# Kernel optimization log

Hardware: AMD Instinct MI355X
Metric: run time of the kernel (lower is better)

The kernel has to match this reference:

```python
import jax, jax.numpy as jnp
import numpy as np

# Model dims (match init_kwargs)
N_P, NV, P, S = 60, 5, 20, 14   # particles, vertices, pf features, sv features
HID, DE, DO, NCLS, BATCH = 60, 20, 24, 2, 512

# Rr/Rs one-hot matrices encode edges (r, s) for r != s with r varying slowest.
# So gather-by-Rr == repeat each node N-1 times, gather-by-Rs == index by senders,
# and scatter-sum by Rr^T == reshape to [B, N, N-1, De] and sum axis 2.
_SENDERS = np.array([s for r in range(N_P) for s in range(N_P) if s != r])


def _lin_params(key, din, dout):
    kw, kb = jax.random.split(key)
    bound = 1.0 / np.sqrt(din)
    w = jax.random.uniform(kw, (din, dout), minval=-bound, maxval=bound, dtype=jnp.float32)
    b = jax.random.uniform(kb, (dout,), minval=-bound, maxval=bound, dtype=jnp.float32)
    return w, b


def setup_inputs() -> dict:
    key = jax.random.key(0)
    ks = jax.random.split(key, 12)
    inp = {
        'x': jax.random.normal(ks[0], (BATCH, P, N_P), dtype=jnp.float32),
        'y': jax.random.normal(ks[1], (BATCH, S, NV), dtype=jnp.float32),
    }
    specs = [('fr', [(2 * P, HID), (HID, HID), (HID, DE)]),
             ('pv', [(S + P, HID), (HID, HID), (HID, DE)]),
             ('fo', [(P + 2 * DE, HID), (HID, HID), (HID, DO)])]
    ki = 2
    for name, dims in specs:
        for j, (di, do) in enumerate(dims, 1):
            w, b = _lin_params(ks[ki], di, do)
            ki += 1
            inp[f'{name}_w{j}'] = w
            inp[f'{name}_b{j}'] = b
    w, b = _lin_params(ks[11], DO, NCLS)
    inp['fc_w'] = w
    inp['fc_b'] = b
    return inp


def _mlp3(h, w1, b1, w2, b2, w3, b3):
    h = jax.nn.relu(h @ w1 + b1)
    h = jax.nn.relu(h @ w2 + b2)
    return jax.nn.relu(h @ w3 + b3)


def reference(x, y, fr_w1, fr_b1, fr_w2, fr_b2, fr_w3, fr_b3,
              pv_w1, pv_b1, pv_w2, pv_b2, pv_w3, pv_b3,
              fo_w1, fo_b1, fo_w2, fo_b2, fo_w3, fo_b3, fc_w, fc_b):
    xt = jnp.swapaxes(x, -1, -2)  # [B, N, P]
    yt = jnp.swapaxes(y, -1, -2)  # [B, Nv, S]
    B = xt.shape[0]

    # particle-particle edge conv (gather via index, scatter-sum via reshape)
    Orr = jnp.repeat(xt, N_P - 1, axis=1)          # [B, Nr, P], receiver features
    Ors = xt[:, _SENDERS]                          # [B, Nr, P], sender features
    E = _mlp3(jnp.concatenate([Orr, Ors], axis=-1),
              fr_w1, fr_b1, fr_w2, fr_b2, fr_w3, fr_b3)  # [B, Nr, De]
    Ebar_pp = E.reshape(B, N_P, N_P - 1, DE).sum(axis=2)  # [B, N, De]

    # particle-vertex edge conv (Rk repeats particles, Rv tiles vertices)
    Ork = jnp.repeat(xt, NV, axis=1)               # [B, Nt, P]
    Orv = jnp.tile(yt, (1, N_P, 1))                # [B, Nt, S]
    E2 = _mlp3(jnp.concatenate([Ork, Orv], axis=-1),
               pv_w1, pv_b1, pv_w2, pv_b2, pv_w3, pv_b3)  # [B, Nt, De]
    Ebar_pv = E2.reshape(B, N_P, NV, DE).sum(axis=2)      # [B, N, De]

    C = jnp.concatenate([xt, Ebar_pp, Ebar_pv], axis=-1)  # [B, N, P + 2*De]
    O = _mlp3(C, fo_w1, fo_b1, fo_w2, fo_b2, fo_w3, fo_b3)  # [B, N, Do]
    return O.sum(axis=-2) @ fc_w + fc_b  # [B, num_classes]
```

## Files before the change

### kernel.cpp

```cpp
#include <hip/hip_runtime.h>

#define BATCH 512
#define NPART 60
#define PFEAT 20
#define SFEAT 14
#define NVTX  5
#define HID   60
#define DE    20
#define DO    24
#define NCLS  2
#define SR    68

typedef _Float16 half8  __attribute__((ext_vector_type(8)));
typedef _Float16 half4v __attribute__((ext_vector_type(4)));
typedef __fp16   fp16x2 __attribute__((ext_vector_type(2)));
typedef float    f32x4  __attribute__((ext_vector_type(4)));

__device__ __forceinline__ half4v pkcvt4(f32x4 a) {
    fp16x2 lo = __builtin_amdgcn_cvt_pkrtz(a[0], a[1]);
    fp16x2 hi = __builtin_amdgcn_cvt_pkrtz(a[2], a[3]);
    half4v r;
    r[0] = (_Float16)lo[0]; r[1] = (_Float16)lo[1];
    r[2] = (_Float16)hi[0]; r[3] = (_Float16)hi[1];
    return r;
}
__device__ __forceinline__ half4v relu4(half4v a) {
#pragma unroll
    for (int j = 0; j < 4; ++j)
        a[j] = (a[j] > (_Float16)0.f) ? a[j] : (_Float16)0.f;
    return a;
}
__device__ __forceinline__ f32x4 bias4(const float* b, int col4, int lim) {
    f32x4 z = {0.f, 0.f, 0.f, 0.f};
    return (col4 < lim) ? *(const f32x4*)(b + col4) : z;
}

__global__ __launch_bounds__(256) void prep_kernel(
    const float* __restrict__ x,
    const float* __restrict__ fr_w1, const float* __restrict__ pv_w1,
    const float* __restrict__ fr_w2, const float* __restrict__ fr_w3,
    const float* __restrict__ pv_w2, const float* __restrict__ pv_w3,
    const float* __restrict__ fo_w1, const float* __restrict__ fo_w2,
    const float* __restrict__ fo_w3,
    _Float16* __restrict__ frW2p, _Float16* __restrict__ frW3p16,
    _Float16* __restrict__ pvW2p, _Float16* __restrict__ pvW3p16,
    _Float16* __restrict__ foW1p, _Float16* __restrict__ foW2p16,
    _Float16* __restrict__ foW3p16,
    _Float16* __restrict__ frW1Ap, _Float16* __restrict__ frW1Bp,
    _Float16* __restrict__ pvW1Ap, _Float16* __restrict__ xp)
{
    if (blockIdx.x < 16) {
        int idx = blockIdx.x*256 + threadIdx.x;
        {
            int j  = idx & 7;
            int L  = (idx >> 3) & 63;
            int kk = (idx >> 9) & 1;
            int u  = idx >> 10;
            int k  = kk*32 + (L >> 4)*8 + j;
            int n  = u*16 + (L & 15);
            bool ok = (k < HID && n < HID);
            frW2p[idx] = (_Float16)(ok ? fr_w2[k*HID + n] : 0.f);
            pvW2p[idx] = (_Float16)(ok ? pv_w2[k*HID + n] : 0.f);
            foW1p[idx] = (_Float16)(ok ? fo_w1[k*HID + n] : 0.f);
        }
        {
            int j  = idx & 3;
            int L  = (idx >> 2) & 63;
            int kt = (idx >> 8) & 3;
            int u  = idx >> 10;
            int k  = kt*16 + (L >> 4)*4 + j;
            int n  = u*16 + (L & 15);
            foW2p16[idx] = (_Float16)((k < HID && n < HID) ? fo_w2[k*HID + n] : 0.f);
        }
        if (idx < 2048) {
            {
                int j  = idx & 3;
                int L  = (idx >> 2) & 63;
                int kt = (idx >> 8) & 3;
                int u  = idx >> 10;
                int k  = kt*16 + (L >> 4)*4 + j;
                int n  = u*16 + (L & 15);
                frW3p16[idx] = (_Float16)((k < HID && n < DE) ? fr_w3[k*DE + n] : 0.f);
                pvW3p16[idx] = (_Float16)((k < HID && n < DE) ? pv_w3[k*DE + n] : 0.f);
                foW3p16[idx] = (_Float16)((k < HID && n < DO) ? fo_w3[k*DO + n] : 0.f);
            }
            {
                int j = idx & 7;
                int L = (idx >> 3) & 63;
                int u = idx >> 9;
                int k = (L >> 4)*8 + j;
                int n = u*16 + (L & 15);
                bool ok = (k < PFEAT && n < HID);
                frW1Ap[idx] = (_Float16)(ok ? fr_w1[k*HID + n] : 0.f);
                frW1Bp[idx] = (_Float16)(ok ? fr_w1[(PFEAT + k)*HID + n] : 0.f);
                pvW1Ap[idx] = (_Float16)(ok ? pv_w1[k*HID + n] : 0.f);
            }
        }
    } else {
        int idx = (blockIdx.x - 16)*256 + threadIdx.x;
        if (idx < BATCH*NPART*4) {
            int p = idx % NPART;
            int t = idx / NPART;
            int q = t & 3;
            int b = t >> 2;
            half8 v;
#pragma unroll
            for (int j = 0; j < 8; ++j) {
                int k = q*8 + j;
                v[j] = (_Float16)((k < PFEAT) ? x[((size_t)b*PFEAT + k)*NPART + p] : 0.f);
            }
            *(half8*)(xp + (size_t)idx*8) = v;
        }
    }
}

__global__ __launch_bounds__(512) void fused_kernel(
    const float* __restrict__ y,
    const float* __restrict__ fr_b1,
    const float* __restrict__ fr_b2, const float* __restrict__ fr_b3,
    const float* __restrict__ pv_w1, const float* __restrict__ pv_b1,
    const float* __restrict__ pv_b2, const float* __restrict__ pv_b3,
    const float* __restrict__ fo_b1, const float* __restrict__ fo_b2,
    const float* __restrict__ fo_b3,
    const float* __restrict__ fcw, const float* __restrict__ fcb,
    const half8*  __restrict__ frw2p, const half4v* __restrict__ frw3p16,
    const half8*  __restrict__ pvw2p, const half4v* __restrict__ pvw3p16,
    const half8*  __restrict__ fow1p, const half4v* __restrict__ fow2p16,
    const half4v* __restrict__ fow3p16,
    const half8*  __restrict__ frw1ap, const half8* __restrict__ frw1bp,
    const half8*  __restrict__ pvw1ap, const _Float16* __restrict__ xp,
    float* __restrict__ out)
{
    __shared__ __align__(16) _Float16 sFrA[NPART*SR];
    __shared__ __align__(16) _Float16 sFrB[NPART*SR];
    __shared__ __align__(16) _Float16 sPvA[NPART*SR];
    __shared__ __align__(16) _Float16 sPvV[NVTX*64];
    __shared__ __align__(16) _Float16 sEpp[NPART*DE];
    __shared__ __align__(16) _Float16 sEpvP[NVTX*NPART*DE];
    __shared__ __align__(16) float    sDsum[4][DO];
    __shared__ __align__(16) float    sBias[7*64];
    _Float16* sCin = sFrA;

    int bb   = blockIdx.x;
    int wv   = threadIdx.x >> 6;
    int lane = threadIdx.x & 63;
    int ml   = lane & 15;
    int q    = lane >> 4;

    {
        if (threadIdx.x < 448) {
            int arr = wv, i = lane;
            float bv = 0.f;
            if      (arr == 0) { if (i < HID) bv = fr_b2[i]; }
            else if (arr == 1) { if (i < DE)  bv = fr_b3[i]; }
            else if (arr == 2) { if (i < HID) bv = pv_b2[i]; }
            else if (arr == 3) { if (i < DE)  bv = pv_b3[i]; }
            else if (arr == 4) { if (i < HID) bv = fo_b1[i]; }
            else if (arr == 5) { if (i < HID) bv = fo_b2[i]; }
            else               { if (i < DO)  bv = fo_b3[i]; }
            sBias[threadIdx.x] = bv;
        }

        int tile = wv & 3;
        int row  = 16*tile + ml;
        int rr   = (row < NPART) ? row : 0;
        half8 bX = *(const half8*)(xp + (((size_t)bb*4 + q)*NPART + rr)*8);
#pragma unroll
        for (int task = 0; task < 2; ++task) {
            const half8* Wt; const float* bset; _Float16* Ot;
            if (wv < 4) {
                if (task == 0) { Wt = frw1ap; bset = fr_b1;  Ot = sFrA; }
                else           { Wt = pvw1ap; bset = nullptr; Ot = sPvA; }
            } else {
                if (task == 1) break;
                Wt = frw1bp; bset = nullptr; Ot = sFrB;
            }
#pragma unroll
            for (int u = 0; u < 4; ++u) {
                half8 w8 = Wt[u*64 + lane];
                f32x4 acc = bset ? bias4(bset, u*16 + 4*q, HID - 3)
                                 : (f32x4){0.f, 0.f, 0.f, 0.f};
                acc = __builtin_amdgcn_mfma_f32_16x16x32_f16(w8, bX, acc, 0, 0, 0);
                if (row < NPART)
                    *(half4v*)(Ot + row*SR + u*16 + 4*q) = pkcvt4(acc);
            }
        }
        for (int idx = threadIdx.x; idx < NVTX*64; idx += 512) {
            int v = idx >> 6;
            int h = idx & 63;
            float a = 0.f;
            if (h < HID) {
                a = pv_b1[h];
#pragma unroll
                for (int f = 0; f < SFEAT; ++f)
                    a += y[((size_t)bb*SFEAT + f)*NVTX + v] * pv_w1[(PFEAT + f)*HID + h];
            }
            sPvV[idx] = (_Float16)a;
        }
    }
    __syncthreads();

    {
        half8  w2r[8];
        half4v w3r[8];
#pragma unroll
        for (int t = 0; t < 8; ++t) w2r[t] = frw2p[t*64 + lane];
#pragma unroll
        for (int t = 0; t < 8; ++t) w3r[t] = frw3p16[t*64 + lane];
#pragma unroll
        for (int t = 0; t < 8; ++t) {
            asm volatile("" : "+v"(w2r[t]));
            asm volatile("" : "+v"(w3r[t]));
        }

        for (int r = wv; r < NPART; r += 8) {
            half8 u8k0 = *(const half8*)(sFrA + r*SR + q*8);
            half8 u8k1 = *(const half8*)(sFrA + r*SR + 32 + q*8);
            float s[2][4];
#pragma unroll
            for (int v = 0; v < 2; ++v)
#pragma unroll
                for (int i = 0; i < 4; ++i) s[v][i] = 0.f;

#pragma unroll
            for (int th = 0; th < 2; ++th) {
                half8 bA[2][2];
                float okf[2];
#pragma unroll
                for (int tl = 0; tl < 2; ++tl) {
                    int edge = 16*(2*th + tl) + ml;
                    bool eok = (edge < NPART-1);
                    okf[tl] = eok ? 1.f : 0.f;
                    int sr = eok ? (edge + (edge >= r)) : 0;
#pragma unroll
                    for (int kk = 0; kk < 2; ++kk) {
                        half8 v8 = *(const half8*)(sFrB + sr*SR + kk*32 + q*8);
                        half8 s8 = (kk ? u8k1 : u8k0) + v8;
#pragma unroll
                        for (int j = 0; j < 8; ++j) {
                            _Float16 vj = s8[j];
                            s8[j] = (vj > (_Float16)0.f) ? vj : (_Float16)0.f;
                        }
                        bA[tl][kk] = s8;
                    }
                }
                f32x4 acc3[2][2];
#pragma unroll
                for (int v = 0; v < 2; ++v) {
                    f32x4 bi = *(const f32x4*)(sBias + 1*64 + v*16 + 4*q);
#pragma unroll
                    for (int tl = 0; tl < 2; ++tl) acc3[v][tl] = bi;
                }
#pragma unroll
                for (int u = 0; u < 4; ++u) {
                    half8 w0 = w2r[u*2 + 0];
                    half8 w1 = w2r[u*2 + 1];
                    f32x4 bi2 = *(const f32x4*)(sBias + 0*64 + u*16 + 4*q);
                    half4v a3u[2];
#pragma unroll
                    for (int tl = 0; tl < 2; ++tl) {
                        f32x4 a = bi2;
                        a = __builtin_amdgcn_mfma_f32_16x16x32_f16(w0, bA[tl][0], a, 0, 0, 0);
                        a = __builtin_amdgcn_mfma_f32_16x16x32_f16(w1, bA[tl][1], a, 0, 0, 0);
                        a3u[tl] = relu4(pkcvt4(a));
                    }
                    half4v w3a = w3r[0*4 + u];
                    half4v w3b = w3r[1*4 + u];
#pragma unroll
                    for (int tl = 0; tl < 2; ++tl) {
                        acc3[0][tl] = __builtin_amdgcn_mfma_f32_16x16x16f16(w3a, a3u[tl], acc3[0][tl], 0, 0, 0);
                        acc3[1][tl] = __builtin_amdgcn_mfma_f32_16x16x16f16(w3b, a3u[tl], acc3[1][tl], 0, 0, 0);
                    }
                }
#pragma unroll
                for (int v = 0; v < 2; ++v)
#pragma unroll
                    for (int tl = 0; tl < 2; ++tl)
#pragma unroll
                        for (int i = 0; i < 4; ++i)
                            s[v][i] = fmaf(fmaxf(acc3[v][tl][i], 0.f), okf[tl], s[v][i]);
            }
#pragma unroll
            for (int v = 0; v < 2; ++v) {
#pragma unroll
                for (int i = 0; i < 4; ++i) {
                    s[v][i] += __shfl_xor(s[v][i], 1);
                    s[v][i] += __shfl_xor(s[v][i], 2);
                    s[v][i] += __shfl_xor(s[v][i], 4);
                    s[v][i] += __shfl_xor(s[v][i], 8);
                }
                int col4 = v*16 + 4*q;
                if (ml == 0 && col4 < DE) {
                    f32x4 o = {s[v][0], s[v][1], s[v][2], s[v][3]};
                    *(half4v*)(sEpp + r*DE + col4) = pkcvt4(o);
                }
            }
        }
    }

    if (wv < NVTX) {
        int gv = wv;
        half8  w2r[8];
        half4v w3r[8];
#pragma unroll
        for (int t = 0; t < 8; ++t) w2r[t] = pvw2p[t*64 + lane];
#pragma unroll
        for (int t = 0; t < 8; ++t) w3r[t] = pvw3p16[t*64 + lane];
#pragma unroll
        for (int t = 0; t < 8; ++t) {
            asm volatile("" : "+v"(w2r[t]));
            asm volatile("" : "+v"(w3r[t]));
        }
        half8 u8k0 = *(const half8*)(sPvV + gv*64 + q*8);
        half8 u8k1 = *(const half8*)(sPvV + gv*64 + 32 + q*8);
#pragma unroll
        for (int th = 0; th < 2; ++th) {
            half8 bA[2][2];
#pragma unroll
            for (int tl = 0; tl < 2; ++tl) {
                int p = 16*(2*th + tl) + ml;
                int sr = (p < NPART) ? p : 0;
#pragma unroll
                for (int kk = 0; kk < 2; ++kk) {
                    half8 v8 = *(const half8*)(sPvA + sr*SR + kk*32 + q*8);
                    half8 s8 = (kk ? u8k1 : u8k0) + v8;
#pragma unroll
                    for (int j = 0; j < 8; ++j) {
                        _Float16 vj = s8[j];
                        s8[j] = (vj > (_Float16)0.f) ? vj : (_Float16)0.f;
                    }
                    bA[tl][kk] = s8;
                }
            }
            f32x4 acc3[2][2];
#pragma unroll
            for (int v = 0; v < 2; ++v) {
                f32x4 bi = *(const f32x4*)(sBias + 3*64 + v*16 + 4*q);
#pragma unroll
                for (int tl = 0; tl < 2; ++tl) acc3[v][tl] = bi;
            }
#pragma unroll
            for (int u = 0; u < 4; ++u) {
                half8 w0 = w2r[u*2 + 0];
                half8 w1 = w2r[u*2 + 1];
                f32x4 bi2 = *(const f32x4*)(sBias + 2*64 + u*16 + 4*q);
                half4v a3u[2];
#pragma unroll
                for (int tl = 0; tl < 2; ++tl) {
                    f32x4 a = bi2;
                    a = __builtin_amdgcn_mfma_f32_16x16x32_f16(w0, bA[tl][0], a, 0, 0, 0);
                    a = __builtin_amdgcn_mfma_f32_16x16x32_f16(w1, bA[tl][1], a, 0, 0, 0);
                    a3u[tl] = relu4(pkcvt4(a));
                }
                half4v w3a = w3r[0*4 + u];
                half4v w3b = w3r[1*4 + u];
#pragma unroll
                for (int tl = 0; tl < 2; ++tl) {
                    acc3[0][tl] = __builtin_amdgcn_mfma_f32_16x16x16f16(w3a, a3u[tl], acc3[0][tl], 0, 0, 0);
                    acc3[1][tl] = __builtin_amdgcn_mfma_f32_16x16x16f16(w3b, a3u[tl], acc3[1][tl], 0, 0, 0);
                }
            }
#pragma unroll
            for (int v = 0; v < 2; ++v) {
                int col4 = v*16 + 4*q;
#pragma unroll
                for (int tl = 0; tl < 2; ++tl) {
                    int p = 16*(2*th + tl) + ml;
                    if (p < NPART && col4 < DE) {
                        half4v hv = relu4(pkcvt4(acc3[v][tl]));
                        *(half4v*)(sEpvP + (gv*NPART + p)*DE + col4) = hv;
                    }
                }
            }
        }
    }
    __syncthreads();

    for (int idx = threadIdx.x; idx < NPART*64; idx += 512) {
        int p = idx >> 6;
        int k = idx & 63;
        _Float16 v;
        if (k < PFEAT) {
            v = xp[(((size_t)bb*4 + (k >> 3))*NPART + p)*8 + (k & 7)];
        } else if (k < PFEAT + DE) {
            v = sEpp[p*DE + (k - PFEAT)];
        } else if (k < PFEAT + 2*DE) {
            int c = k - PFEAT - DE;
            float s = 0.f;
#pragma unroll
            for (int g5 = 0; g5 < NVTX; ++g5)
                s += (float)sEpvP[(g5*NPART + p)*DE + c];
            v = (_Float16)s;
        } else {
            v = (_Float16)0.f;
        }
        sCin[p*SR + k] = v;
    }
    __syncthreads();

    if (wv < 4) {
        int p = 16*wv + ml;
        int sp = (p < NPART) ? p : 0;
        half8 bC[2];
#pragma unroll
        for (int kk = 0; kk < 2; ++kk)
            bC[kk] = *(const half8*)(sCin + sp*SR + kk*32 + q*8);

        f32x4 acc1[4];
#pragma unroll
        for (int u = 0; u < 4; ++u) {
            acc1[u] = *(const f32x4*)(sBias + 4*64 + u*16 + 4*q);
            acc1[u] = __builtin_amdgcn_mfma_f32_16x16x32_f16(fow1p[(u*2 + 0)*64 + lane], bC[0], acc1[u], 0, 0, 0);
            acc1[u] = __builtin_amdgcn_mfma_f32_16x16x32_f16(fow1p[(u*2 + 1)*64 + lane], bC[1], acc1[u], 0, 0, 0);
        }
        half4v a2[4];
#pragma unroll
        for (int u = 0; u < 4; ++u) a2[u] = relu4(pkcvt4(acc1[u]));

        f32x4 acc2[4];
#pragma unroll
        for (int u = 0; u < 4; ++u) {
            acc2[u] = *(const f32x4*)(sBias + 5*64 + u*16 + 4*q);
#pragma unroll
            for (int kt = 0; kt < 4; ++kt)
                acc2[u] = __builtin_amdgcn_mfma_f32_16x16x16f16(fow2p16[(u*4 + kt)*64 + lane], a2[kt], acc2[u], 0, 0, 0);
        }
        half4v a3[4];
#pragma unroll
        for (int u = 0; u < 4; ++u) a3[u] = relu4(pkcvt4(acc2[u]));

        f32x4 acc3[2];
#pragma unroll
        for (int v = 0; v < 2; ++v) {
            acc3[v] = *(const f32x4*)(sBias + 6*64 + v*16 + 4*q);
#pragma unroll
            for (int u = 0; u < 4; ++u)
                acc3[v] = __builtin_amdgcn_mfma_f32_16x16x16f16(fow3p16[(v*4 + u)*64 + lane], a3[u], acc3[v], 0, 0, 0);
        }
#pragma unroll
        for (int v = 0; v < 2; ++v) {
            float s[4];
            bool ok = p < NPART;
#pragma unroll
            for (int i = 0; i < 4; ++i)
                s[i] = ok ? fmaxf(acc3[v][i], 0.f) : 0.f;
#pragma unroll
            for (int i = 0; i < 4; ++i) {
                s[i] += __shfl_xor(s[i], 1);
                s[i] += __shfl_xor(s[i], 2);
                s[i] += __shfl_xor(s[i], 4);
                s[i] += __shfl_xor(s[i], 8);
            }
            int col4 = v*16 + 4*q;
            if (ml == 0 && col4 < DO) {
                f32x4 o = {s[0], s[1], s[2], s[3]};
                *(f32x4*)(sDsum[wv] + col4) = o;
            }
        }
    }
    __syncthreads();

    if (wv == 0) {
        float tot = 0.f;
        if (lane < DO) {
#pragma unroll
            for (int w4 = 0; w4 < 4; ++w4) tot += sDsum[w4][lane];
        }
        float p0 = (lane < DO) ? tot * fcw[lane*NCLS + 0] : 0.f;
        float p1 = (lane < DO) ? tot * fcw[lane*NCLS + 1] : 0.f;
#pragma unroll
        for (int d = 1; d <= 16; d <<= 1) {
            p0 += __shfl_xor(p0, d);
            p1 += __shfl_xor(p1, d);
        }
        if (lane == 0) {
            out[bb*NCLS + 0] = p0 + fcb[0];
            out[bb*NCLS + 1] = p1 + fcb[1];
        }
    }
}

extern "C" void kernel_launch(void* const* d_in, const int* in_sizes, int n_in,
                              void* d_out, int out_size, void* d_ws, size_t ws_size,
                              hipStream_t stream)
{
    const float* x     = (const float*)d_in[0];
    const float* y     = (const float*)d_in[1];
    const float* fr_w1 = (const float*)d_in[2];
    const float* fr_b1 = (const float*)d_in[3];
    const float* fr_w2 = (const float*)d_in[4];
    const float* fr_b2 = (const float*)d_in[5];
    const float* fr_w3 = (const float*)d_in[6];
    const float* fr_b3 = (const float*)d_in[7];
    const float* pv_w1 = (const float*)d_in[8];
    const float* pv_b1 = (const float*)d_in[9];
    const float* pv_w2 = (const float*)d_in[10];
    const float* pv_b2 = (const float*)d_in[11];
    const float* pv_w3 = (const float*)d_in[12];
    const float* pv_b3 = (const float*)d_in[13];
    const float* fo_w1 = (const float*)d_in[14];
    const float* fo_b1 = (const float*)d_in[15];
    const float* fo_w2 = (const float*)d_in[16];
    const float* fo_b2 = (const float*)d_in[17];
    const float* fo_w3 = (const float*)d_in[18];
    const float* fo_b3 = (const float*)d_in[19];
    const float* fc_w  = (const float*)d_in[20];
    const float* fc_b  = (const float*)d_in[21];
    float* out = (float*)d_out;

    char* wsb = (char*)d_ws;
    size_t off = 0;
    auto alloc = [&](size_t bytes) { char* p = wsb + off; off += (bytes + 255) & ~(size_t)255; return p; };

    _Float16* frW2p   = (_Float16*)alloc(4096*2);
    _Float16* frW3p16 = (_Float16*)alloc(2048*2);
    _Float16* pvW2p   = (_Float16*)alloc(4096*2);
    _Float16* pvW3p16 = (_Float16*)alloc(2048*2);
    _Float16* foW1p   = (_Float16*)alloc(4096*2);
    _Float16* foW2p16 = (_Float16*)alloc(4096*2);
    _Float16* foW3p16 = (_Float16*)alloc(2048*2);
    _Float16* frW1Ap  = (_Float16*)alloc(2048*2);
    _Float16* frW1Bp  = (_Float16*)alloc(2048*2);
    _Float16* pvW1Ap  = (_Float16*)alloc(2048*2);
    _Float16* xp      = (_Float16*)alloc((size_t)BATCH*NPART*32*2);

    int xblocks = (BATCH*NPART*4 + 255)/256;
    prep_kernel<<<16 + xblocks, 256, 0, stream>>>(
        x, fr_w1, pv_w1,
        fr_w2, fr_w3, pv_w2, pv_w3, fo_w1, fo_w2, fo_w3,
        frW2p, frW3p16, pvW2p, pvW3p16, foW1p, foW2p16, foW3p16,
        frW1Ap, frW1Bp, pvW1Ap, xp);

    fused_kernel<<<BATCH, 512, 0, stream>>>(
        y, fr_b1, fr_b2, fr_b3,
        pv_w1, pv_b1, pv_b2, pv_b3,
        fo_b1, fo_b2, fo_b3, fc_w, fc_b,
        (const half8*)frW2p, (const half4v*)frW3p16,
        (const half8*)pvW2p, (const half4v*)pvW3p16,
        (const half8*)foW1p, (const half4v*)foW2p16, (const half4v*)foW3p16,
        (const half8*)frW1Ap, (const half8*)frW1Bp,
        (const half8*)pvW1Ap, xp,
        out);
}
```

Measured before the change: 150.6 us.

## Fold biases into padded weight rows via a constant-one homogeneous channel

Biases are folded into the zero-padded K rows of the packed fp16 weight matrices. Each activation carries a constant 1 at feature index HID (or PFEAT for the input), so every layer's MFMA adds the bias itself and re-emits the 1 for the next layer. This removes the shared-memory bias table, its per-block fill, and the per-tile bias loads into accumulators. In exchange, biases are rounded to fp16, and correctness relies on the 1-channel surviving ReLU and on the padding lanes being laid out consistently across every layer and stage.

```diff
diff --git a/kernel.cpp b/kernel.cpp
--- a/kernel.cpp
+++ b/kernel.cpp
@@ -30,18 +30,18 @@
         a[j] = (a[j] > (_Float16)0.f) ? a[j] : (_Float16)0.f;
     return a;
 }
-__device__ __forceinline__ f32x4 bias4(const float* b, int col4, int lim) {
-    f32x4 z = {0.f, 0.f, 0.f, 0.f};
-    return (col4 < lim) ? *(const f32x4*)(b + col4) : z;
-}
 
 __global__ __launch_bounds__(256) void prep_kernel(
     const float* __restrict__ x,
-    const float* __restrict__ fr_w1, const float* __restrict__ pv_w1,
-    const float* __restrict__ fr_w2, const float* __restrict__ fr_w3,
-    const float* __restrict__ pv_w2, const float* __restrict__ pv_w3,
-    const float* __restrict__ fo_w1, const float* __restrict__ fo_w2,
-    const float* __restrict__ fo_w3,
+    const float* __restrict__ fr_w1, const float* __restrict__ fr_b1,
+    const float* __restrict__ pv_w1,
+    const float* __restrict__ fr_w2, const float* __restrict__ fr_b2,
+    const float* __restrict__ fr_w3, const float* __restrict__ fr_b3,
+    const float* __restrict__ pv_w2, const float* __restrict__ pv_b2,
+    const float* __restrict__ pv_w3, const float* __restrict__ pv_b3,
+    const float* __restrict__ fo_w1, const float* __restrict__ fo_b1,
+    const float* __restrict__ fo_w2, const float* __restrict__ fo_b2,
+    const float* __restrict__ fo_w3, const float* __restrict__ fo_b3,
     _Float16* __restrict__ frW2p, _Float16* __restrict__ frW3p16,
     _Float16* __restrict__ pvW2p, _Float16* __restrict__ pvW3p16,
     _Float16* __restrict__ foW1p, _Float16* __restrict__ foW2p16,
@@ -58,10 +58,18 @@
             int u  = idx >> 10;
             int k  = kk*32 + (L >> 4)*8 + j;
             int n  = u*16 + (L & 15);
-            bool ok = (k < HID && n < HID);
-            frW2p[idx] = (_Float16)(ok ? fr_w2[k*HID + n] : 0.f);
-            pvW2p[idx] = (_Float16)(ok ? pv_w2[k*HID + n] : 0.f);
-            foW1p[idx] = (_Float16)(ok ? fo_w1[k*HID + n] : 0.f);
+            float v2f = 0.f, v2p = 0.f, v1o = 0.f;
+            if (k < HID && n < HID) {
+                v2f = fr_w2[k*HID + n];
+                v2p = pv_w2[k*HID + n];
+                v1o = fo_w1[k*HID + n];
+            } else if (k == HID) {
+                if (n < HID)      { v2f = fr_b2[n]; v2p = pv_b2[n]; v1o = fo_b1[n]; }
+                else if (n == HID){ v2f = 1.f;      v2p = 1.f;      v1o = 1.f; }
+            }
+            frW2p[idx] = (_Float16)v2f;
+            pvW2p[idx] = (_Float16)v2p;
+            foW1p[idx] = (_Float16)v1o;
         }
         {
             int j  = idx & 3;
@@ -70,7 +78,13 @@
             int u  = idx >> 10;
             int k  = kt*16 + (L >> 4)*4 + j;
             int n  = u*16 + (L & 15);
-            foW2p16[idx] = (_Float16)((k < HID && n < HID) ? fo_w2[k*HID + n] : 0.f);
+            float v = 0.f;
+            if (k < HID && n < HID)        v = fo_w2[k*HID + n];
+            else if (k == HID) {
+                if (n < HID)       v = fo_b2[n];
+                else if (n == HID) v = 1.f;
+            }
+            foW2p16[idx] = (_Float16)v;
         }
         if (idx < 2048) {
             {
@@ -80,9 +94,17 @@
                 int u  = idx >> 10;
                 int k  = kt*16 + (L >> 4)*4 + j;
                 int n  = u*16 + (L & 15);
-                frW3p16[idx] = (_Float16)((k < HID && n < DE) ? fr_w3[k*DE + n] : 0.f);
-                pvW3p16[idx] = (_Float16)((k < HID && n < DE) ? pv_w3[k*DE + n] : 0.f);
-                foW3p16[idx] = (_Float16)((k < HID && n < DO) ? fo_w3[k*DO + n] : 0.f);
+                float vf = 0.f, vp = 0.f, vo = 0.f;
+                if (k < HID) {
+                    if (n < DE) { vf = fr_w3[k*DE + n]; vp = pv_w3[k*DE + n]; }
+                    if (n < DO)   vo = fo_w3[k*DO + n];
+                } else if (k == HID) {
+                    if (n < DE) { vf = fr_b3[n]; vp = pv_b3[n]; }
+                    if (n < DO)   vo = fo_b3[n];
+                }
+                frW3p16[idx] = (_Float16)vf;
+                pvW3p16[idx] = (_Float16)vp;
+                foW3p16[idx] = (_Float16)vo;
             }
             {
                 int j = idx & 7;
@@ -90,10 +112,18 @@
                 int u = idx >> 9;
                 int k = (L >> 4)*8 + j;
                 int n = u*16 + (L & 15);
-                bool ok = (k < PFEAT && n < HID);
-                frW1Ap[idx] = (_Float16)(ok ? fr_w1[k*HID + n] : 0.f);
-                frW1Bp[idx] = (_Float16)(ok ? fr_w1[(PFEAT + k)*HID + n] : 0.f);
-                pvW1Ap[idx] = (_Float16)(ok ? pv_w1[k*HID + n] : 0.f);
+                float va = 0.f, vb = 0.f, vpv = 0.f;
+                if (k < PFEAT && n < HID) {
+                    va  = fr_w1[k*HID + n];
+                    vb  = fr_w1[(PFEAT + k)*HID + n];
+                    vpv = pv_w1[k*HID + n];
+                } else if (k == PFEAT) {
+                    if (n < HID)       va = fr_b1[n];
+                    else if (n == HID) va = 1.f;
+                }
+                frW1Ap[idx] = (_Float16)va;
+                frW1Bp[idx] = (_Float16)vb;
+                pvW1Ap[idx] = (_Float16)vpv;
             }
         }
     } else {
@@ -107,7 +137,10 @@
 #pragma unroll
             for (int j = 0; j < 8; ++j) {
                 int k = q*8 + j;
-                v[j] = (_Float16)((k < PFEAT) ? x[((size_t)b*PFEAT + k)*NPART + p] : 0.f);
+                float f = 0.f;
+                if (k < PFEAT)       f = x[((size_t)b*PFEAT + k)*NPART + p];
+                else if (k == PFEAT) f = 1.f;
+                v[j] = (_Float16)f;
             }
             *(half8*)(xp + (size_t)idx*8) = v;
         }
@@ -116,12 +149,7 @@
 
 __global__ __launch_bounds__(512) void fused_kernel(
     const float* __restrict__ y,
-    const float* __restrict__ fr_b1,
-    const float* __restrict__ fr_b2, const float* __restrict__ fr_b3,
     const float* __restrict__ pv_w1, const float* __restrict__ pv_b1,
-    const float* __restrict__ pv_b2, const float* __restrict__ pv_b3,
-    const float* __restrict__ fo_b1, const float* __restrict__ fo_b2,
-    const float* __restrict__ fo_b3,
     const float* __restrict__ fcw, const float* __restrict__ fcb,
     const half8*  __restrict__ frw2p, const half4v* __restrict__ frw3p16,
     const half8*  __restrict__ pvw2p, const half4v* __restrict__ pvw3p16,
@@ -138,8 +166,9 @@
     __shared__ __align__(16) _Float16 sEpp[NPART*DE];
     __shared__ __align__(16) _Float16 sEpvP[NVTX*NPART*DE];
     __shared__ __align__(16) float    sDsum[4][DO];
-    __shared__ __align__(16) float    sBias[7*64];
     _Float16* sCin = sFrA;
+
+    const f32x4 z4 = {0.f, 0.f, 0.f, 0.f};
 
     int bb   = blockIdx.x;
     int wv   = threadIdx.x >> 6;
@@ -148,38 +177,24 @@
     int q    = lane >> 4;
 
     {
-        if (threadIdx.x < 448) {
-            int arr = wv, i = lane;
-            float bv = 0.f;
-            if      (arr == 0) { if (i < HID) bv = fr_b2[i]; }
-            else if (arr == 1) { if (i < DE)  bv = fr_b3[i]; }
-            else if (arr == 2) { if (i < HID) bv = pv_b2[i]; }
-            else if (arr == 3) { if (i < DE)  bv = pv_b3[i]; }
-            else if (arr == 4) { if (i < HID) bv = fo_b1[i]; }
-            else if (arr == 5) { if (i < HID) bv = fo_b2[i]; }
-            else               { if (i < DO)  bv = fo_b3[i]; }
-            sBias[threadIdx.x] = bv;
-        }
-
         int tile = wv & 3;
         int row  = 16*tile + ml;
         int rr   = (row < NPART) ? row : 0;
         half8 bX = *(const half8*)(xp + (((size_t)bb*4 + q)*NPART + rr)*8);
 #pragma unroll
         for (int task = 0; task < 2; ++task) {
-            const half8* Wt; const float* bset; _Float16* Ot;
+            const half8* Wt; _Float16* Ot;
             if (wv < 4) {
-                if (task == 0) { Wt = frw1ap; bset = fr_b1;  Ot = sFrA; }
-                else           { Wt = pvw1ap; bset = nullptr; Ot = sPvA; }
+                if (task == 0) { Wt = frw1ap; Ot = sFrA; }
+                else           { Wt = pvw1ap; Ot = sPvA; }
             } else {
                 if (task == 1) break;
-                Wt = frw1bp; bset = nullptr; Ot = sFrB;
+                Wt = frw1bp; Ot = sFrB;
             }
 #pragma unroll
             for (int u = 0; u < 4; ++u) {
                 half8 w8 = Wt[u*64 + lane];
-                f32x4 acc = bset ? bias4(bset, u*16 + 4*q, HID - 3)
-                                 : (f32x4){0.f, 0.f, 0.f, 0.f};
+                f32x4 acc = z4;
                 acc = __builtin_amdgcn_mfma_f32_16x16x32_f16(w8, bX, acc, 0, 0, 0);
                 if (row < NPART)
                     *(half4v*)(Ot + row*SR + u*16 + 4*q) = pkcvt4(acc);
@@ -188,12 +203,14 @@
         for (int idx = threadIdx.x; idx < NVTX*64; idx += 512) {
             int v = idx >> 6;
             int h = idx & 63;
-            float a = 0.f;
+            float a;
             if (h < HID) {
                 a = pv_b1[h];
 #pragma unroll
                 for (int f = 0; f < SFEAT; ++f)
                     a += y[((size_t)bb*SFEAT + f)*NVTX + v] * pv_w1[(PFEAT + f)*HID + h];
+            } else {
+                a = (h == HID) ? 1.f : 0.f;
             }
             sPvV[idx] = (_Float16)a;
         }
@@ -246,20 +263,17 @@
                 }
                 f32x4 acc3[2][2];
 #pragma unroll
-                for (int v = 0; v < 2; ++v) {
-                    f32x4 bi = *(const f32x4*)(sBias + 1*64 + v*16 + 4*q);
-#pragma unroll
-                    for (int tl = 0; tl < 2; ++tl) acc3[v][tl] = bi;
-                }
+                for (int v = 0; v < 2; ++v)
+#pragma unroll
+                    for (int tl = 0; tl < 2; ++tl) acc3[v][tl] = z4;
 #pragma unroll
                 for (int u = 0; u < 4; ++u) {
                     half8 w0 = w2r[u*2 + 0];
                     half8 w1 = w2r[u*2 + 1];
-                    f32x4 bi2 = *(const f32x4*)(sBias + 0*64 + u*16 + 4*q);
                     half4v a3u[2];
 #pragma unroll
                     for (int tl = 0; tl < 2; ++tl) {
-                        f32x4 a = bi2;
+                        f32x4 a = z4;
                         a = __builtin_amdgcn_mfma_f32_16x16x32_f16(w0, bA[tl][0], a, 0, 0, 0);
                         a = __builtin_amdgcn_mfma_f32_16x16x32_f16(w1, bA[tl][1], a, 0, 0, 0);
                         a3u[tl] = relu4(pkcvt4(a));
@@ -334,20 +348,17 @@
             }
             f32x4 acc3[2][2];
 #pragma unroll
-            for (int v = 0; v < 2; ++v) {
-                f32x4 bi = *(const f32x4*)(sBias + 3*64 + v*16 + 4*q);
-#pragma unroll
-                for (int tl = 0; tl < 2; ++tl) acc3[v][tl] = bi;
-            }
+            for (int v = 0; v < 2; ++v)
+#pragma unroll
+                for (int tl = 0; tl < 2; ++tl) acc3[v][tl] = z4;
 #pragma unroll
             for (int u = 0; u < 4; ++u) {
                 half8 w0 = w2r[u*2 + 0];
                 half8 w1 = w2r[u*2 + 1];
-                f32x4 bi2 = *(const f32x4*)(sBias + 2*64 + u*16 + 4*q);
                 half4v a3u[2];
 #pragma unroll
                 for (int tl = 0; tl < 2; ++tl) {
-                    f32x4 a = bi2;
+                    f32x4 a = z4;
                     a = __builtin_amdgcn_mfma_f32_16x16x32_f16(w0, bA[tl][0], a, 0, 0, 0);
                     a = __builtin_amdgcn_mfma_f32_16x16x32_f16(w1, bA[tl][1], a, 0, 0, 0);
                     a3u[tl] = relu4(pkcvt4(a));
@@ -392,7 +403,7 @@
                 s += (float)sEpvP[(g5*NPART + p)*DE + c];
             v = (_Float16)s;
         } else {
-            v = (_Float16)0.f;
+            v = (k == HID) ? (_Float16)1.f : (_Float16)0.f;
         }
         sCin[p*SR + k] = v;
     }
@@ -409,7 +420,7 @@
         f32x4 acc1[4];
 #pragma unroll
         for (int u = 0; u < 4; ++u) {
-            acc1[u] = *(const f32x4*)(sBias + 4*64 + u*16 + 4*q);
+            acc1[u] = z4;
             acc1[u] = __builtin_amdgcn_mfma_f32_16x16x32_f16(fow1p[(u*2 + 0)*64 + lane], bC[0], acc1[u], 0, 0, 0);
             acc1[u] = __builtin_amdgcn_mfma_f32_16x16x32_f16(fow1p[(u*2 + 1)*64 + lane], bC[1], acc1[u], 0, 0, 0);
         }
@@ -420,7 +431,7 @@
         f32x4 acc2[4];
 #pragma unroll
         for (int u = 0; u < 4; ++u) {
-            acc2[u] = *(const f32x4*)(sBias + 5*64 + u*16 + 4*q);
+            acc2[u] = z4;
 #pragma unroll
             for (int kt = 0; kt < 4; ++kt)
                 acc2[u] = __builtin_amdgcn_mfma_f32_16x16x16f16(fow2p16[(u*4 + kt)*64 + lane], a2[kt], acc2[u], 0, 0, 0);
@@ -432,7 +443,7 @@
         f32x4 acc3[2];
 #pragma unroll
         for (int v = 0; v < 2; ++v) {
-            acc3[v] = *(const f32x4*)(sBias + 6*64 + v*16 + 4*q);
+            acc3[v] = z4;
 #pragma unroll
             for (int u = 0; u < 4; ++u)
                 acc3[v] = __builtin_amdgcn_mfma_f32_16x16x16f16(fow3p16[(v*4 + u)*64 + lane], a3[u], acc3[v], 0, 0, 0);
@@ -526,15 +537,15 @@
 
     int xblocks = (BATCH*NPART*4 + 255)/256;
     prep_kernel<<<16 + xblocks, 256, 0, stream>>>(
-        x, fr_w1, pv_w1,
-        fr_w2, fr_w3, pv_w2, pv_w3, fo_w1, fo_w2, fo_w3,
+        x, fr_w1, fr_b1, pv_w1,
+        fr_w2, fr_b2, fr_w3, fr_b3,
+        pv_w2, pv_b2, pv_w3, pv_b3,
+        fo_w1, fo_b1, fo_w2, fo_b2, fo_w3, fo_b3,
         frW2p, frW3p16, pvW2p, pvW3p16, foW1p, foW2p16, foW3p16,
         frW1Ap, frW1Bp, pvW1Ap, xp);
 
     fused_kernel<<<BATCH, 512, 0, stream>>>(
-        y, fr_b1, fr_b2, fr_b3,
-        pv_w1, pv_b1, pv_b2, pv_b3,
-        fo_b1, fo_b2, fo_b3, fc_w, fc_b,
+        y, pv_w1, pv_b1, fc_w, fc_b,
         (const half8*)frW2p, (const half4v*)frW3p16,
         (const half8*)pvW2p, (const half4v*)pvW3p16,
         (const half8*)foW1p, (const half4v*)foW2p16, (const half4v*)foW3p16,
```

Result: faster. 145.3 us (-3.5%).
